# Kernel tuning notes

Measured on AMD Instinct MI355X. Metric: run time of the kernel, lower is better.

## Reference

```python
import jax, jax.numpy as jnp
import numpy as np

N = 10000      # nodes
E = 160000     # edges
B = 16         # graphs in batch
F_NODE = 42
F_EDGE = 12
D = 256        # hidden_dim
H = 4          # heads
C = D // H     # per-head channels = 64
L = 5          # num_layers
NEG_SLOPE = 0.2  # GATConv leaky_relu slope


def layernorm(x, g, b, eps=1e-5):
    mu = jnp.mean(x, axis=-1, keepdims=True)
    var = jnp.var(x, axis=-1, keepdims=True)
    return (x - mu) * jax.lax.rsqrt(var + eps) * g + b


def setup_inputs() -> dict:
    key = jax.random.key(0)
    ks = jax.random.split(key, 20)
    def w(i, shape, scale=0.05):
        return jax.random.normal(ks[i], shape, dtype=jnp.float32) * scale
    return {
        "x": jax.random.normal(ks[0], (N, F_NODE), dtype=jnp.float32),
        "edge_attr": jax.random.normal(ks[1], (E, F_EDGE), dtype=jnp.float32),
        "edge_index": jax.random.randint(ks[2], (2, E), 0, N),
        "batch": jnp.sort(jax.random.randint(ks[3], (N,), 0, B)),
        # node / edge encoders
        "enc_w": w(4, (F_NODE, D)), "enc_b": jnp.zeros((D,), jnp.float32),
        "eenc_w": w(5, (F_EDGE, D)), "eenc_b": jnp.zeros((D,), jnp.float32),
        # stacked GAT layer params [L, ...]
        "gat_w": w(6, (L, D, D)),          # lin_src == lin_dst (shared in PyG for Tensor input)
        "att_src": w(7, (L, H, C)),
        "att_dst": w(8, (L, H, C)),
        "att_edge": w(9, (L, H, C)),
        "gat_ew": w(10, (L, D, D)),        # lin_edge
        "gat_b": jnp.zeros((L, D), jnp.float32),
        "ln_g": jnp.ones((L, D), jnp.float32),
        "ln_b": jnp.zeros((L, D), jnp.float32),
        # attention pooling gate MLP
        "gate_w1": w(11, (D, D)), "gate_b1": jnp.zeros((D,), jnp.float32),
        "gate_w2": w(12, (D, 1)), "gate_b2": jnp.zeros((1,), jnp.float32),
        # MLP readout (mlp_layers=2)
        "ro_w1": w(13, (D, D)), "ro_b1": jnp.zeros((D,), jnp.float32),
        "ro_w2": w(14, (D, D)), "ro_b2": jnp.zeros((D,), jnp.float32),
    }


def reference(x, edge_index, edge_attr, batch, enc_w, enc_b, eenc_w, eenc_b,
              gat_w, att_src, att_dst, att_edge, gat_ew, gat_b, ln_g, ln_b,
              gate_w1, gate_b1, gate_w2, gate_b2, ro_w1, ro_b1, ro_w2, ro_b2):
    src0, dst0 = edge_index[0], edge_index[1]

    # encoders (dropout is identity at eval)
    h = jax.nn.relu(x @ enc_w + enc_b)                      # [N, D]
    e = jax.nn.relu(edge_attr @ eenc_w + eenc_b)            # [E, D]

    # GATConv add_self_loops with fill_value='mean': self-loop edge feature is
    # the mean of incoming edge features per destination node.
    esum = jax.ops.segment_sum(e, dst0, num_segments=N)
    cnt = jax.ops.segment_sum(jnp.ones((E,), e.dtype), dst0, num_segments=N)
    e_self = esum / jnp.maximum(cnt, 1.0)[:, None]
    e_full = jnp.concatenate([e, e_self], axis=0)           # [E+N, D]
    loops = jnp.arange(N)
    src = jnp.concatenate([src0, loops])
    dst = jnp.concatenate([dst0, loops])

    for l in range(L):
        xh = (h @ gat_w[l]).reshape(N, H, C)                # [N, H, C]
        a_s = jnp.einsum('nhc,hc->nh', xh, att_src[l])      # [N, H]
        a_d = jnp.einsum('nhc,hc->nh', xh, att_dst[l])
        eh = (e_full @ gat_ew[l]).reshape(-1, H, C)         # [E+N, H, C]
        a_e = jnp.einsum('ehc,hc->eh', eh, att_edge[l])
        alpha = jax.nn.leaky_relu(a_s[src] + a_d[dst] + a_e, NEG_SLOPE)  # [E+N, H]
        # softmax over incoming edges per destination node (stable)
        m = jax.lax.stop_gradient(jax.ops.segment_max(alpha, dst, num_segments=N))
        ex = jnp.exp(alpha - m[dst])
        den = jax.ops.segment_sum(ex, dst, num_segments=N)
        attn = ex / den[dst]                                # [E+N, H]
        msg = xh[src] * attn[:, :, None]                    # [E+N, H, C]
        out = jax.ops.segment_sum(msg, dst, num_segments=N).reshape(N, D) + gat_b[l]
        out = jax.nn.relu(layernorm(out, ln_g[l], ln_b[l]))
        h = h + out                                         # residual

    # GlobalAttention pooling: softmax(gate_nn(h)) per graph, weighted sum
    gate = (jax.nn.relu(h @ gate_w1 + gate_b1) @ gate_w2 + gate_b2)[:, 0]  # [N]
    gm = jax.lax.stop_gradient(jax.ops.segment_max(gate, batch, num_segments=B))
    ge = jnp.exp(gate - gm[batch])
    gd = jax.ops.segment_sum(ge, batch, num_segments=B)
    wgt = ge / gd[batch]
    g_embed = jax.ops.segment_sum(h * wgt[:, None], batch, num_segments=B)  # [B, D]

    # MLP readout
    return jax.nn.relu(g_embed @ ro_w1 + ro_b1) @ ro_w2 + ro_b2  # [B, D]
```

## Files before the change

### kernel.cpp

```cpp
#include <hip/hip_runtime.h>
#include <math.h>

#define DD 256
#define HH 4
#define CC 64
#define LL 5
#define NEG_SLOPE 0.2f
#define LH 20
#define WCAP 192

typedef __bf16 bf16x8 __attribute__((ext_vector_type(8)));
typedef __bf16 bf16x4 __attribute__((ext_vector_type(4)));
typedef float f32x4 __attribute__((ext_vector_type(4)));

static __device__ __forceinline__ float lrelu(float x) {
    return x > 0.0f ? x : NEG_SLOPE * x;
}

__global__ __launch_bounds__(256) void wproj_kernel(
    const float* __restrict__ gat_ew, const float* __restrict__ att_edge,
    float* __restrict__ wproj) {
    int l = blockIdx.x;
    int k = threadIdx.x;
    const float* W = gat_ew + (size_t)l * DD * DD;
    const float* att = att_edge + l * DD;
    for (int hh = 0; hh < HH; ++hh) {
        float s = 0.f;
        #pragma unroll
        for (int c = 0; c < CC; ++c)
            s += W[k * DD + hh * CC + c] * att[hh * CC + c];
        wproj[k * LH + l * HH + hh] = s;
    }
}

__global__ __launch_bounds__(256) void pack_edge_frags_kernel(
    const float* __restrict__ eenc_w, const float* __restrict__ eenc_b,
    const float* __restrict__ wproj, __bf16* __restrict__ wfe,
    __bf16* __restrict__ wfp) {
    int tid = threadIdx.x;
    for (int idx = tid; idx < 16 * 64; idx += 256) {
        int t = idx >> 6, lane = idx & 63;
        int q = lane >> 4, r15 = lane & 15;
        int col = t * 16 + r15;
        #pragma unroll
        for (int j = 0; j < 8; ++j) {
            int k = q * 8 + j;
            float v = (k < 12) ? eenc_w[k * 256 + col]
                               : (k == 12 ? eenc_b[col] : 0.f);
            wfe[(size_t)idx * 8 + j] = (__bf16)v;
        }
    }
    for (int idx = tid; idx < 16 * 64; idx += 256) {
        int sidx = idx >> 6, lane = idx & 63;
        int s = sidx >> 1, t2 = sidx & 1;
        int q = lane >> 4, r15 = lane & 15;
        int col = t2 * 16 + r15;
        #pragma unroll
        for (int j = 0; j < 8; ++j) {
            int k = s * 32 + q * 8 + j;
            float v = (col < LH) ? wproj[k * LH + col] : 0.f;
            wfp[(size_t)idx * 8 + j] = (__bf16)v;
        }
    }
}

__global__ __launch_bounds__(256) void wswizzle_kernel(
    const float* __restrict__ gat_w, const float* __restrict__ gate_w1,
    __bf16* __restrict__ wf) {
    int b = blockIdx.x;
    int l = b >> 5;
    int rem = b & 31;
    int y = rem >> 3, ks = rem & 7;
    int tid = threadIdx.x;
    int t = tid >> 6, lane = tid & 63;
    int q = lane >> 4, r15 = lane & 15;
    const float* W = (l < 5) ? (gat_w + (size_t)l * DD * DD) : gate_w1;
    size_t obase = (((size_t)b * 4 + t) * 64 + lane) * 8;
    int kbase = ks * 32 + q * 8;
    int col = y * 64 + t * 16 + r15;
    #pragma unroll
    for (int j = 0; j < 8; ++j)
        wf[obase + j] = (__bf16)W[(size_t)(kbase + j) * DD + col];
}

__global__ __launch_bounds__(256) void encoder_kernel(
    const float* __restrict__ x, const float* __restrict__ enc_w,
    const float* __restrict__ enc_b, float* __restrict__ h,
    __bf16* __restrict__ hbf, int N) {
    int n = blockIdx.x;
    int tid = threadIdx.x;
    __shared__ float xs[42];
    if (tid < 42) xs[tid] = x[(size_t)n * 42 + tid];
    __syncthreads();
    float acc = enc_b[tid];
    #pragma unroll
    for (int f = 0; f < 42; ++f) acc += xs[f] * enc_w[f * DD + tid];
    float v = fmaxf(acc, 0.f);
    h[(size_t)n * DD + tid] = v;
    hbf[(size_t)n * DD + tid] = (__bf16)v;
}

__global__ __launch_bounds__(256) void edge_mfma_kernel(
    const float* __restrict__ edge_attr, const __bf16* __restrict__ wfe,
    const __bf16* __restrict__ wfp, const int* __restrict__ pos,
    float* __restrict__ a_e_csr, int E) {
    __shared__ __bf16 sm[4][16][264];
    int tid = threadIdx.x;
    int w = tid >> 6, lane = tid & 63;
    int q = lane >> 4, r15 = lane & 15;
    int eb = blockIdx.x * 64 + w * 16;
    int e = eb + r15;
    int ec = min(e, E - 1);
    bf16x8 a1;
    #pragma unroll
    for (int j = 0; j < 8; ++j) a1[j] = (__bf16)0.f;
    if (q == 0) {
        const float4* p = (const float4*)(edge_attr + (size_t)ec * 12);
        float4 p0 = p[0], p1 = p[1];
        a1[0] = (__bf16)p0.x; a1[1] = (__bf16)p0.y; a1[2] = (__bf16)p0.z; a1[3] = (__bf16)p0.w;
        a1[4] = (__bf16)p1.x; a1[5] = (__bf16)p1.y; a1[6] = (__bf16)p1.z; a1[7] = (__bf16)p1.w;
    } else if (q == 1) {
        float4 p2 = *(const float4*)(edge_attr + (size_t)ec * 12 + 8);
        a1[0] = (__bf16)p2.x; a1[1] = (__bf16)p2.y; a1[2] = (__bf16)p2.z; a1[3] = (__bf16)p2.w;
        a1[4] = (__bf16)1.0f;
    }
    const bf16x8* wfeP = (const bf16x8*)wfe;
    f32x4 zero = (f32x4){0.f, 0.f, 0.f, 0.f};
    #pragma unroll
    for (int t = 0; t < 16; ++t) {
        bf16x8 bfr = wfeP[t * 64 + lane];
        f32x4 c = __builtin_amdgcn_mfma_f32_16x16x32_bf16(a1, bfr, zero, 0, 0, 0);
        int col = t * 16 + r15;
        #pragma unroll
        for (int r = 0; r < 4; ++r)
            sm[w][q * 4 + r][col] = (__bf16)fmaxf(c[r], 0.f);
    }
    const bf16x8* wfpP = (const bf16x8*)wfp;
    f32x4 c2[2];
    c2[0] = zero; c2[1] = zero;
    #pragma unroll
    for (int s = 0; s < 8; ++s) {
        bf16x8 a2 = *(const bf16x8*)&sm[w][r15][s * 32 + q * 8];
        #pragma unroll
        for (int t2 = 0; t2 < 2; ++t2)
            c2[t2] = __builtin_amdgcn_mfma_f32_16x16x32_bf16(
                a2, wfpP[(s * 2 + t2) * 64 + lane], c2[t2], 0, 0, 0);
    }
    #pragma unroll
    for (int t2 = 0; t2 < 2; ++t2) {
        int col = t2 * 16 + r15;
        if (col >= LH) continue;
        #pragma unroll
        for (int r = 0; r < 4; ++r) {
            int e2 = eb + q * 4 + r;
            if (e2 < E) {
                int pk = pos[e2];
                a_e_csr[(size_t)pk * LH + col] = c2[t2][r];
            }
        }
    }
}

__global__ void deg_kernel(const int* __restrict__ dst, int* __restrict__ deg, int E) {
    int e = blockIdx.x * 256 + threadIdx.x;
    if (e < E) atomicAdd(&deg[dst[e]], 1);
}

__global__ void self_ae_kernel(const int* __restrict__ row_ptr,
                               float* __restrict__ a_e_csr, int N, int E) {
    int i = blockIdx.x * 256 + threadIdx.x;
    if (i >= N * LH) return;
    int n = i / LH;
    int j = i % LH;
    int rs = row_ptr[n], re = row_ptr[n + 1];
    float s = 0.f;
    for (int k = rs; k < re; ++k)
        s += a_e_csr[(size_t)k * LH + j];
    a_e_csr[(size_t)(E + n) * LH + j] = s / (float)max(re - rs, 1);
}

__global__ __launch_bounds__(1024) void scan_kernel(const int* __restrict__ deg,
                                                    int* __restrict__ row_ptr,
                                                    int* __restrict__ cursor, int n) {
    __shared__ int wsum[16];
    __shared__ int carry_s;
    int tid = threadIdx.x;
    int w = tid >> 6, lane = tid & 63;
    if (tid == 0) carry_s = 0;
    __syncthreads();
    for (int base = 0; base < n; base += 1024) {
        int i = base + tid;
        int v = (i < n) ? deg[i] : 0;
        int carry = carry_s;
        int s = v;
        #pragma unroll
        for (int off = 1; off < 64; off <<= 1) {
            int t = __shfl_up(s, off, 64);
            if (lane >= off) s += t;
        }
        if (lane == 63) wsum[w] = s;
        __syncthreads();
        if (w == 0 && lane < 16) {
            int ws = wsum[lane];
            #pragma unroll
            for (int off = 1; off < 16; off <<= 1) {
                int t = __shfl_up(ws, off, 64);
                if (lane >= off) ws += t;
            }
            wsum[lane] = ws;
        }
        __syncthreads();
        int waveoff = (w == 0) ? 0 : wsum[w - 1];
        if (i < n) {
            int ex = carry + waveoff + s - v;
            row_ptr[i] = ex;
            cursor[i] = ex;
        }
        __syncthreads();
        if (tid == 0) carry_s = carry + wsum[15];
        __syncthreads();
    }
    if (tid == 0) row_ptr[n] = carry_s;
}

__global__ void scatter_kernel(const int* __restrict__ src, const int* __restrict__ dst,
                               int* __restrict__ cursor, int* __restrict__ csr_src,
                               int* __restrict__ pos, int E) {
    int e = blockIdx.x * 256 + threadIdx.x;
    if (e >= E) return;
    int d = dst[e];
    int pk = atomicAdd(&cursor[d], 1);
    csr_src[pk] = src[e];
    pos[e] = pk;
}

__global__ __launch_bounds__(256) void gemm_mfma_kernel(
    const __bf16* __restrict__ hbf, const __bf16* __restrict__ wf,
    __bf16* __restrict__ xhbf, int M,
    const float* __restrict__ att_src, const float* __restrict__ att_dst,
    float* __restrict__ a_s, float* __restrict__ a_d,
    const float* __restrict__ bias, const float* __restrict__ gate_w2,
    const float* __restrict__ gate_b2, float* __restrict__ gate_out) {
    int tid = threadIdx.x;
    int w = tid >> 6, lane = tid & 63;
    int q = lane >> 4, r15 = lane & 15;
    int m0 = blockIdx.x * 64;
    int y2 = blockIdx.y;
    int arow = m0 + w * 16 + r15;
    int arowc = min(arow, M - 1);
    const __bf16* ap = hbf + (size_t)arowc * DD + q * 8;
    const bf16x8* wfP = (const bf16x8*)wf;
    f32x4 acc[8];
    #pragma unroll
    for (int g = 0; g < 8; ++g) acc[g] = (f32x4){0.f, 0.f, 0.f, 0.f};
    #pragma unroll
    for (int ks = 0; ks < 8; ++ks) {
        bf16x8 a = *(const bf16x8*)(ap + ks * 32);
        #pragma unroll
        for (int g = 0; g < 8; ++g) {
            int y = y2 * 2 + (g >> 2);
            int t = g & 3;
            bf16x8 b = wfP[(size_t)(((y * 8 + ks) * 4) + t) * 64 + lane];
            acc[g] = __builtin_amdgcn_mfma_f32_16x16x32_bf16(a, b, acc[g], 0, 0, 0);
        }
    }
    if (xhbf) {
        #pragma unroll
        for (int g = 0; g < 8; ++g) {
            int col = (y2 * 8 + g) * 16 + r15;
            #pragma unroll
            for (int r = 0; r < 4; ++r) {
                int rc = m0 + w * 16 + q * 4 + r;
                if (rc < M) xhbf[(size_t)rc * DD + col] = (__bf16)acc[g][r];
            }
        }
    }
    if (att_src) {
        #pragma unroll
        for (int r = 0; r < 4; ++r) {
            float ps0 = 0.f, pd0 = 0.f, ps1 = 0.f, pd1 = 0.f;
            #pragma unroll
            for (int g = 0; g < 8; ++g) {
                int col = (y2 * 8 + g) * 16 + r15;
                float v = acc[g][r];
                if (g < 4) { ps0 += v * att_src[col]; pd0 += v * att_dst[col]; }
                else       { ps1 += v * att_src[col]; pd1 += v * att_dst[col]; }
            }
            #pragma unroll
            for (int mask = 1; mask < 16; mask <<= 1) {
                ps0 += __shfl_xor(ps0, mask, 64);
                pd0 += __shfl_xor(pd0, mask, 64);
                ps1 += __shfl_xor(ps1, mask, 64);
                pd1 += __shfl_xor(pd1, mask, 64);
            }
            int rc = m0 + w * 16 + q * 4 + r;
            if (r15 == 0 && rc < M) {
                a_s[rc * HH + y2 * 2 + 0] = ps0;
                a_d[rc * HH + y2 * 2 + 0] = pd0;
                a_s[rc * HH + y2 * 2 + 1] = ps1;
                a_d[rc * HH + y2 * 2 + 1] = pd1;
            }
        }
    }
    if (gate_w2) {
        #pragma unroll
        for (int r = 0; r < 4; ++r) {
            float pg = 0.f;
            #pragma unroll
            for (int g = 0; g < 8; ++g) {
                int col = (y2 * 8 + g) * 16 + r15;
                pg += fmaxf(acc[g][r] + bias[col], 0.f) * gate_w2[col];
            }
            #pragma unroll
            for (int mask = 1; mask < 16; mask <<= 1) pg += __shfl_xor(pg, mask, 64);
            int rc = m0 + w * 16 + q * 4 + r;
            if (r15 == 0 && rc < M) {
                float add = pg + (y2 == 0 ? gate_b2[0] : 0.f);
                atomicAdd(&gate_out[rc], add);
            }
        }
    }
}

__global__ __launch_bounds__(256) void gat_message7_kernel(
    const __bf16* __restrict__ xhbf, const float* __restrict__ a_s,
    const float* __restrict__ a_d, const float* __restrict__ a_e,
    const int* __restrict__ row_ptr, const int* __restrict__ csr_src,
    const float* __restrict__ gat_b,
    const float* __restrict__ ln_g, const float* __restrict__ ln_b,
    float* __restrict__ h, __bf16* __restrict__ hbf, int N, int E) {
    __shared__ float lws[4][WCAP * 4];
    __shared__ int lsrc[4][WCAP];
    int tid = threadIdx.x;
    int w = tid >> 6, lane = tid & 63;
    int n = blockIdx.x * 4 + w;
    if (n >= N) return;
    int hh = lane >> 4, j = lane & 15;
    int rs = row_ptr[n], re = row_ptr[n + 1];
    int deg = re - rs;
    float adn = a_d[n * HH + hh];
    float al_self = lrelu(a_s[n * HH + hh] + adn + a_e[(size_t)(E + n) * LH + hh]);
    float m = al_self, den = 0.f;
    for (int k = rs + j; k < re; k += 16) {
        int kk = k - rs;
        int s = csr_src[k];
        float a = lrelu(a_s[s * HH + hh] + adn + a_e[(size_t)k * LH + hh]);
        if (kk < WCAP) {
            lws[w][kk * 4 + hh] = a;
            if (hh == 0) lsrc[w][kk] = s;
        }
        float mn = fmaxf(m, a);
        den = den * __expf(m - mn) + __expf(a - mn);
        m = mn;
    }
    #pragma unroll
    for (int off = 1; off < 16; off <<= 1) {
        float m2 = __shfl_xor(m, off, 64);
        float d2 = __shfl_xor(den, off, 64);
        float mn = fmaxf(m, m2);
        den = den * __expf(m - mn) + d2 * __expf(m2 - mn);
        m = mn;
    }
    den += __expf(al_self - m);
    float inv_den = 1.0f / den;
    int cap = min(deg, WCAP);
    for (int kk = j; kk < cap; kk += 16)
        lws[w][kk * 4 + hh] = __expf(lws[w][kk * 4 + hh] - m) * inv_den;
    float wself = __expf(al_self - m) * inv_den;
    bf16x4 xsb = *((const bf16x4*)(xhbf + (size_t)n * DD) + lane);
    float4 acc;
    acc.x = wself * (float)xsb[0]; acc.y = wself * (float)xsb[1];
    acc.z = wself * (float)xsb[2]; acc.w = wself * (float)xsb[3];
    int k = rs;
    for (; k + 1 < re; k += 2) {
        int kk0 = k - rs, kk1 = kk0 + 1;
        int s0, s1_;
        float w0, w1;
        if (kk1 < WCAP) {
            s0 = lsrc[w][kk0]; s1_ = lsrc[w][kk1];
            w0 = lws[w][kk0 * 4 + hh]; w1 = lws[w][kk1 * 4 + hh];
        } else {
            s0 = csr_src[k]; s1_ = csr_src[k + 1];
            w0 = (kk0 < WCAP) ? lws[w][kk0 * 4 + hh]
               : __expf(lrelu(a_s[s0 * HH + hh] + adn + a_e[(size_t)k * LH + hh]) - m) * inv_den;
            w1 = __expf(lrelu(a_s[s1_ * HH + hh] + adn + a_e[(size_t)(k + 1) * LH + hh]) - m) * inv_den;
        }
        bf16x4 x0 = *((const bf16x4*)(xhbf + (size_t)s0 * DD) + lane);
        bf16x4 x1 = *((const bf16x4*)(xhbf + (size_t)s1_ * DD) + lane);
        acc.x += w0 * (float)x0[0] + w1 * (float)x1[0];
        acc.y += w0 * (float)x0[1] + w1 * (float)x1[1];
        acc.z += w0 * (float)x0[2] + w1 * (float)x1[2];
        acc.w += w0 * (float)x0[3] + w1 * (float)x1[3];
    }
    if (k < re) {
        int kk0 = k - rs;
        int s0;
        float w0;
        if (kk0 < WCAP) { s0 = lsrc[w][kk0]; w0 = lws[w][kk0 * 4 + hh]; }
        else {
            s0 = csr_src[k];
            w0 = __expf(lrelu(a_s[s0 * HH + hh] + adn + a_e[(size_t)k * LH + hh]) - m) * inv_den;
        }
        bf16x4 x0 = *((const bf16x4*)(xhbf + (size_t)s0 * DD) + lane);
        acc.x += w0 * (float)x0[0]; acc.y += w0 * (float)x0[1];
        acc.z += w0 * (float)x0[2]; acc.w += w0 * (float)x0[3];
    }
    float4 gb = *((const float4*)gat_b + lane);
    float4 val;
    val.x = acc.x + gb.x; val.y = acc.y + gb.y;
    val.z = acc.z + gb.z; val.w = acc.w + gb.w;
    float s1 = val.x + val.y + val.z + val.w;
    float s2 = val.x * val.x + val.y * val.y + val.z * val.z + val.w * val.w;
    #pragma unroll
    for (int off = 1; off < 64; off <<= 1) {
        s1 += __shfl_xor(s1, off, 64);
        s2 += __shfl_xor(s2, off, 64);
    }
    float mu = s1 * (1.0f / DD);
    float var = s2 * (1.0f / DD) - mu * mu;
    float rstd = rsqrtf(var + 1e-5f);
    float4 lg = *((const float4*)ln_g + lane);
    float4 lb = *((const float4*)ln_b + lane);
    float4 nv;
    nv.x = fmaxf((val.x - mu) * rstd * lg.x + lb.x, 0.f);
    nv.y = fmaxf((val.y - mu) * rstd * lg.y + lb.y, 0.f);
    nv.z = fmaxf((val.z - mu) * rstd * lg.z + lb.z, 0.f);
    nv.w = fmaxf((val.w - mu) * rstd * lg.w + lb.w, 0.f);
    float4* hp = (float4*)(h + (size_t)n * DD) + lane;
    float4 hv = *hp;
    hv.x += nv.x; hv.y += nv.y; hv.z += nv.z; hv.w += nv.w;
    *hp = hv;
    bf16x4 hb;
    hb[0] = (__bf16)hv.x; hb[1] = (__bf16)hv.y;
    hb[2] = (__bf16)hv.z; hb[3] = (__bf16)hv.w;
    *((bf16x4*)(hbf + (size_t)n * DD) + lane) = hb;
}

__global__ __launch_bounds__(256) void gseg_kernel(
    const float* __restrict__ gate, const int* __restrict__ batch,
    float* __restrict__ gmax, float* __restrict__ gden, int N) {
    int b = blockIdx.x;
    int tid = threadIdx.x;
    __shared__ int bounds[2];
    if (tid < 2) {
        int target = b + tid;
        int lo = 0, hi = N;
        while (lo < hi) {
            int mid = (lo + hi) >> 1;
            if (batch[mid] < target) lo = mid + 1; else hi = mid;
        }
        bounds[tid] = lo;
    }
    __syncthreads();
    int s0 = bounds[0], s1 = bounds[1];
    __shared__ float red[256];
    float m = -1e30f;
    for (int i = s0 + tid; i < s1; i += 256) m = fmaxf(m, gate[i]);
    red[tid] = m;
    __syncthreads();
    for (int off = 128; off; off >>= 1) {
        if (tid < off) red[tid] = fmaxf(red[tid], red[tid + off]);
        __syncthreads();
    }
    float gm = red[0];
    __syncthreads();
    float s = 0.f;
    for (int i = s0 + tid; i < s1; i += 256) s += __expf(gate[i] - gm);
    red[tid] = s;
    __syncthreads();
    for (int off = 128; off; off >>= 1) {
        if (tid < off) red[tid] += red[tid + off];
        __syncthreads();
    }
    if (tid == 0) {
        gmax[b] = gm;
        gden[b] = red[0];
    }
}

#define POOL_CHUNK 32
__global__ __launch_bounds__(256) void pool_scatter_kernel(
    const float* __restrict__ h, const float* __restrict__ gate,
    const float* __restrict__ gmax, const float* __restrict__ gden,
    const int* __restrict__ batch, float* __restrict__ g_embed, int N) {
    int i0 = blockIdx.x * POOL_CHUNK;
    int d = threadIdx.x;
    int iend = min(i0 + POOL_CHUNK, N);
    float acc = 0.f;
    int cur = batch[i0];
    for (int i = i0; i < iend; ++i) {
        int b = batch[i];
        if (b != cur) {
            atomicAdd(&g_embed[cur * DD + d], acc);
            acc = 0.f;
            cur = b;
        }
        float wgt = __expf(gate[i] - gmax[b]) / gden[b];
        acc += wgt * h[(size_t)i * DD + d];
    }
    atomicAdd(&g_embed[cur * DD + d], acc);
}

__global__ __launch_bounds__(256) void readout_kernel(
    const float* __restrict__ g_embed, const float* __restrict__ w1,
    const float* __restrict__ b1, const float* __restrict__ w2,
    const float* __restrict__ b2, float* __restrict__ out) {
    int b = blockIdx.x;
    int tid = threadIdx.x;
    __shared__ float gvec[256];
    __shared__ float hid[256];
    gvec[tid] = g_embed[b * DD + tid];
    __syncthreads();
    float hv = b1[tid];
    for (int k = 0; k < DD; ++k) hv += gvec[k] * w1[k * DD + tid];
    hid[tid] = fmaxf(hv, 0.f);
    __syncthreads();
    float o = b2[tid];
    for (int t = 0; t < DD; ++t) o += hid[t] * w2[t * DD + tid];
    out[b * DD + tid] = o;
}

extern "C" void kernel_launch(void* const* d_in, const int* in_sizes, int n_in,
                              void* d_out, int out_size, void* d_ws, size_t ws_size,
                              hipStream_t stream) {
    const float* x        = (const float*)d_in[0];
    const float* edge_attr= (const float*)d_in[1];
    const int*   edge_idx = (const int*)d_in[2];
    const int*   batch    = (const int*)d_in[3];
    const float* enc_w    = (const float*)d_in[4];
    const float* enc_b    = (const float*)d_in[5];
    const float* eenc_w   = (const float*)d_in[6];
    const float* eenc_b   = (const float*)d_in[7];
    const float* gat_w    = (const float*)d_in[8];
    const float* att_src  = (const float*)d_in[9];
    const float* att_dst  = (const float*)d_in[10];
    const float* att_edge = (const float*)d_in[11];
    const float* gat_ew   = (const float*)d_in[12];
    const float* gat_b    = (const float*)d_in[13];
    const float* ln_g     = (const float*)d_in[14];
    const float* ln_b     = (const float*)d_in[15];
    const float* gate_w1  = (const float*)d_in[16];
    const float* gate_b1  = (const float*)d_in[17];
    const float* gate_w2  = (const float*)d_in[18];
    const float* gate_b2  = (const float*)d_in[19];
    const float* ro_w1    = (const float*)d_in[20];
    const float* ro_b1    = (const float*)d_in[21];
    const float* ro_w2    = (const float*)d_in[22];
    const float* ro_b2    = (const float*)d_in[23];
    float* out = (float*)d_out;

    const int N = in_sizes[0] / 42;
    const int E = in_sizes[1] / 12;
    const int B = out_size / DD;

    char* p = (char*)d_ws;
    auto alloc = [&](size_t bytes) {
        char* r = p;
        p += (bytes + 255) & ~(size_t)255;
        return (void*)r;
    };
    float*  h       = (float*)alloc((size_t)N * DD * 4);
    __bf16* hbf     = (__bf16*)alloc((size_t)N * DD * 2);
    __bf16* xhbf    = (__bf16*)alloc((size_t)N * DD * 2);
    float*  a_s     = (float*)alloc((size_t)N * HH * 4);
    float*  a_d     = (float*)alloc((size_t)N * HH * 4);
    float*  a_e_csr = (float*)alloc((size_t)(E + N) * LH * 4);
    float*  wproj   = (float*)alloc((size_t)DD * LH * 4);
    __bf16* wfe     = (__bf16*)alloc((size_t)16 * 64 * 8 * 2);
    __bf16* wfp     = (__bf16*)alloc((size_t)16 * 64 * 8 * 2);
    __bf16* wf      = (__bf16*)alloc((size_t)6 * DD * DD * 2);
    float*  gate    = (float*)alloc((size_t)N * 4);
    float*  g_embed = (float*)alloc((size_t)B * DD * 4);
    float*  gmax    = (float*)alloc((size_t)B * 4);
    float*  gden    = (float*)alloc((size_t)B * 4);
    int* deg        = (int*)alloc((size_t)N * 4);
    int* row_ptr    = (int*)alloc((size_t)(N + 1) * 4);
    int* cursor     = (int*)alloc((size_t)N * 4);
    int* csr_src    = (int*)alloc((size_t)E * 4);
    int* pos        = (int*)alloc((size_t)E * 4);

    const int* src_arr = edge_idx;
    const int* dst_arr = edge_idx + E;

    hipMemsetAsync(deg, 0, (size_t)N * 4, stream);
    hipMemsetAsync(g_embed, 0, (size_t)B * DD * 4, stream);
    hipMemsetAsync(gate, 0, (size_t)N * 4, stream);

    wproj_kernel<<<LL, 256, 0, stream>>>(gat_ew, att_edge, wproj);
    pack_edge_frags_kernel<<<1, 256, 0, stream>>>(eenc_w, eenc_b, wproj, wfe, wfp);
    wswizzle_kernel<<<192, 256, 0, stream>>>(gat_w, gate_w1, wf);
    encoder_kernel<<<N, 256, 0, stream>>>(x, enc_w, enc_b, h, hbf, N);
    deg_kernel<<<(E + 255) / 256, 256, 0, stream>>>(dst_arr, deg, E);
    scan_kernel<<<1, 1024, 0, stream>>>(deg, row_ptr, cursor, N);
    scatter_kernel<<<(E + 255) / 256, 256, 0, stream>>>(
        src_arr, dst_arr, cursor, csr_src, pos, E);
    edge_mfma_kernel<<<(E + 63) / 64, 256, 0, stream>>>(
        edge_attr, wfe, wfp, pos, a_e_csr, E);
    self_ae_kernel<<<(N * LH + 255) / 256, 256, 0, stream>>>(
        row_ptr, a_e_csr, N, E);

    dim3 ggrid((N + 63) / 64, 2);
    for (int l = 0; l < LL; ++l) {
        gemm_mfma_kernel<<<ggrid, 256, 0, stream>>>(
            hbf, wf + (size_t)l * DD * DD, xhbf, N,
            att_src + l * DD, att_dst + l * DD, a_s, a_d,
            nullptr, nullptr, nullptr, nullptr);
        gat_message7_kernel<<<(N + 3) / 4, 256, 0, stream>>>(
            xhbf, a_s, a_d, a_e_csr + l * HH, row_ptr, csr_src,
            gat_b + l * DD, ln_g + l * DD, ln_b + l * DD, h, hbf, N, E);
    }

    gemm_mfma_kernel<<<ggrid, 256, 0, stream>>>(
        hbf, wf + (size_t)5 * DD * DD, nullptr, N,
        nullptr, nullptr, nullptr, nullptr,
        gate_b1, gate_w2, gate_b2, gate);
    gseg_kernel<<<B, 256, 0, stream>>>(gate, batch, gmax, gden, N);
    pool_scatter_kernel<<<(N + POOL_CHUNK - 1) / POOL_CHUNK, 256, 0, stream>>>(
        h, gate, gmax, gden, batch, g_embed, N);
    readout_kernel<<<B, 256, 0, stream>>>(g_embed, ro_w1, ro_b1, ro_w2, ro_b2, out);
}
```

Baseline: 428.7 us.

## Merge independent setup kernels into one mega launch and fuse scan with packing

Combines wproj, weight swizzle, degree counting, node encoder and two memsets into a single kernel that dispatches work by block index. Also folds the edge-fragment packing into a second block of the scan kernel. The aim is to cut launch overhead and the serialization gaps between small setup kernels. The trade-off is branch-heavy block dispatch, and the encoder path now uses __syncthreads inside a divergent-by-block branch, which is safe because it diverges per block.

```diff
diff --git a/kernel.cpp b/kernel.cpp
--- a/kernel.cpp
+++ b/kernel.cpp
@@ -17,87 +17,164 @@
     return x > 0.0f ? x : NEG_SLOPE * x;
 }
 
-__global__ __launch_bounds__(256) void wproj_kernel(
+__global__ __launch_bounds__(256) void mega_setup_kernel(
     const float* __restrict__ gat_ew, const float* __restrict__ att_edge,
-    float* __restrict__ wproj) {
-    int l = blockIdx.x;
-    int k = threadIdx.x;
-    const float* W = gat_ew + (size_t)l * DD * DD;
-    const float* att = att_edge + l * DD;
-    for (int hh = 0; hh < HH; ++hh) {
-        float s = 0.f;
-        #pragma unroll
-        for (int c = 0; c < CC; ++c)
-            s += W[k * DD + hh * CC + c] * att[hh * CC + c];
-        wproj[k * LH + l * HH + hh] = s;
-    }
-}
-
-__global__ __launch_bounds__(256) void pack_edge_frags_kernel(
+    float* __restrict__ wproj,
+    const float* __restrict__ gat_w, const float* __restrict__ gate_w1,
+    __bf16* __restrict__ wf,
+    const int* __restrict__ dst_arr, int* __restrict__ deg,
+    const float* __restrict__ x, const float* __restrict__ enc_w,
+    const float* __restrict__ enc_b, float* __restrict__ h,
+    __bf16* __restrict__ hbf,
+    float* __restrict__ g_embed, float* __restrict__ gate_out,
+    int N, int E, int B) {
+    int blk = blockIdx.x;
+    int tid = threadIdx.x;
+    int EB = (E + 255) >> 8;
+    if (blk < 5) {
+        int l = blk;
+        int k = tid;
+        const float* W = gat_ew + (size_t)l * DD * DD;
+        const float* att = att_edge + l * DD;
+        for (int hh = 0; hh < HH; ++hh) {
+            float s = 0.f;
+            #pragma unroll
+            for (int c = 0; c < CC; ++c)
+                s += W[k * DD + hh * CC + c] * att[hh * CC + c];
+            wproj[k * LH + l * HH + hh] = s;
+        }
+        return;
+    }
+    blk -= 5;
+    if (blk < 192) {
+        int b = blk;
+        int l = b >> 5;
+        int rem = b & 31;
+        int y = rem >> 3, ks = rem & 7;
+        int t = tid >> 6, lane = tid & 63;
+        int q = lane >> 4, r15 = lane & 15;
+        const float* W = (l < 5) ? (gat_w + (size_t)l * DD * DD) : gate_w1;
+        size_t obase = (((size_t)b * 4 + t) * 64 + lane) * 8;
+        int kbase = ks * 32 + q * 8;
+        int col = y * 64 + t * 16 + r15;
+        #pragma unroll
+        for (int j = 0; j < 8; ++j)
+            wf[obase + j] = (__bf16)W[(size_t)(kbase + j) * DD + col];
+        return;
+    }
+    blk -= 192;
+    if (blk < EB) {
+        int e = blk * 256 + tid;
+        if (e < E) atomicAdd(&deg[dst_arr[e]], 1);
+        return;
+    }
+    blk -= EB;
+    if (blk < N) {
+        int n = blk;
+        __shared__ float xs[42];
+        if (tid < 42) xs[tid] = x[(size_t)n * 42 + tid];
+        __syncthreads();
+        float acc = enc_b[tid];
+        #pragma unroll
+        for (int f = 0; f < 42; ++f) acc += xs[f] * enc_w[f * DD + tid];
+        float v = fmaxf(acc, 0.f);
+        h[(size_t)n * DD + tid] = v;
+        hbf[(size_t)n * DD + tid] = (__bf16)v;
+        return;
+    }
+    blk -= N;
+    if (blk == 0) {
+        for (int i = tid; i < B * DD; i += 256) g_embed[i] = 0.f;
+        return;
+    }
+    for (int i = tid; i < N; i += 256) gate_out[i] = 0.f;
+}
+
+__global__ __launch_bounds__(1024) void scan_pack_kernel(
+    const int* __restrict__ deg, int* __restrict__ row_ptr,
+    int* __restrict__ cursor, int n,
     const float* __restrict__ eenc_w, const float* __restrict__ eenc_b,
     const float* __restrict__ wproj, __bf16* __restrict__ wfe,
     __bf16* __restrict__ wfp) {
     int tid = threadIdx.x;
-    for (int idx = tid; idx < 16 * 64; idx += 256) {
-        int t = idx >> 6, lane = idx & 63;
-        int q = lane >> 4, r15 = lane & 15;
-        int col = t * 16 + r15;
-        #pragma unroll
-        for (int j = 0; j < 8; ++j) {
-            int k = q * 8 + j;
-            float v = (k < 12) ? eenc_w[k * 256 + col]
-                               : (k == 12 ? eenc_b[col] : 0.f);
-            wfe[(size_t)idx * 8 + j] = (__bf16)v;
-        }
-    }
-    for (int idx = tid; idx < 16 * 64; idx += 256) {
-        int sidx = idx >> 6, lane = idx & 63;
-        int s = sidx >> 1, t2 = sidx & 1;
-        int q = lane >> 4, r15 = lane & 15;
-        int col = t2 * 16 + r15;
-        #pragma unroll
-        for (int j = 0; j < 8; ++j) {
-            int k = s * 32 + q * 8 + j;
-            float v = (col < LH) ? wproj[k * LH + col] : 0.f;
-            wfp[(size_t)idx * 8 + j] = (__bf16)v;
-        }
-    }
-}
-
-__global__ __launch_bounds__(256) void wswizzle_kernel(
-    const float* __restrict__ gat_w, const float* __restrict__ gate_w1,
-    __bf16* __restrict__ wf) {
-    int b = blockIdx.x;
-    int l = b >> 5;
-    int rem = b & 31;
-    int y = rem >> 3, ks = rem & 7;
-    int tid = threadIdx.x;
-    int t = tid >> 6, lane = tid & 63;
-    int q = lane >> 4, r15 = lane & 15;
-    const float* W = (l < 5) ? (gat_w + (size_t)l * DD * DD) : gate_w1;
-    size_t obase = (((size_t)b * 4 + t) * 64 + lane) * 8;
-    int kbase = ks * 32 + q * 8;
-    int col = y * 64 + t * 16 + r15;
-    #pragma unroll
-    for (int j = 0; j < 8; ++j)
-        wf[obase + j] = (__bf16)W[(size_t)(kbase + j) * DD + col];
-}
-
-__global__ __launch_bounds__(256) void encoder_kernel(
-    const float* __restrict__ x, const float* __restrict__ enc_w,
-    const float* __restrict__ enc_b, float* __restrict__ h,
-    __bf16* __restrict__ hbf, int N) {
-    int n = blockIdx.x;
-    int tid = threadIdx.x;
-    __shared__ float xs[42];
-    if (tid < 42) xs[tid] = x[(size_t)n * 42 + tid];
+    if (blockIdx.x == 1) {
+        {
+            int idx = tid;
+            int t = idx >> 6, lane = idx & 63;
+            int q = lane >> 4, r15 = lane & 15;
+            int col = t * 16 + r15;
+            #pragma unroll
+            for (int j = 0; j < 8; ++j) {
+                int k = q * 8 + j;
+                float v = (k < 12) ? eenc_w[k * 256 + col]
+                                   : (k == 12 ? eenc_b[col] : 0.f);
+                wfe[(size_t)idx * 8 + j] = (__bf16)v;
+            }
+        }
+        {
+            int idx = tid;
+            int sidx = idx >> 6, lane = idx & 63;
+            int s = sidx >> 1, t2 = sidx & 1;
+            int q = lane >> 4, r15 = lane & 15;
+            int col = t2 * 16 + r15;
+            #pragma unroll
+            for (int j = 0; j < 8; ++j) {
+                int k = s * 32 + q * 8 + j;
+                float v = (col < LH) ? wproj[k * LH + col] : 0.f;
+                wfp[(size_t)idx * 8 + j] = (__bf16)v;
+            }
+        }
+        return;
+    }
+    __shared__ int wsum[16];
+    __shared__ int carry_s;
+    int w = tid >> 6, lane = tid & 63;
+    if (tid == 0) carry_s = 0;
     __syncthreads();
-    float acc = enc_b[tid];
-    #pragma unroll
-    for (int f = 0; f < 42; ++f) acc += xs[f] * enc_w[f * DD + tid];
-    float v = fmaxf(acc, 0.f);
-    h[(size_t)n * DD + tid] = v;
-    hbf[(size_t)n * DD + tid] = (__bf16)v;
+    for (int base = 0; base < n; base += 1024) {
+        int i = base + tid;
+        int v = (i < n) ? deg[i] : 0;
+        int carry = carry_s;
+        int s = v;
+        #pragma unroll
+        for (int off = 1; off < 64; off <<= 1) {
+            int t = __shfl_up(s, off, 64);
+            if (lane >= off) s += t;
+        }
+        if (lane == 63) wsum[w] = s;
+        __syncthreads();
+        if (w == 0 && lane < 16) {
+            int ws = wsum[lane];
+            #pragma unroll
+            for (int off = 1; off < 16; off <<= 1) {
+                int t = __shfl_up(ws, off, 64);
+                if (lane >= off) ws += t;
+            }
+            wsum[lane] = ws;
+        }
+        __syncthreads();
+        int waveoff = (w == 0) ? 0 : wsum[w - 1];
+        if (i < n) {
+            int ex = carry + waveoff + s - v;
+            row_ptr[i] = ex;
+            cursor[i] = ex;
+        }
+        __syncthreads();
+        if (tid == 0) carry_s = carry + wsum[15];
+        __syncthreads();
+    }
+    if (tid == 0) row_ptr[n] = carry_s;
+}
+
+__global__ void scatter_kernel(const int* __restrict__ src, const int* __restrict__ dst,
+                               int* __restrict__ cursor, int* __restrict__ csr_src,
+                               int* __restrict__ pos, int E) {
+    int e = blockIdx.x * 256 + threadIdx.x;
+    if (e >= E) return;
+    int d = dst[e];
+    int pk = atomicAdd(&cursor[d], 1);
+    csr_src[pk] = src[e];
+    pos[e] = pk;
 }
 
 __global__ __launch_bounds__(256) void edge_mfma_kernel(
@@ -161,11 +238,6 @@
     }
 }
 
-__global__ void deg_kernel(const int* __restrict__ dst, int* __restrict__ deg, int E) {
-    int e = blockIdx.x * 256 + threadIdx.x;
-    if (e < E) atomicAdd(&deg[dst[e]], 1);
-}
-
 __global__ void self_ae_kernel(const int* __restrict__ row_ptr,
                                float* __restrict__ a_e_csr, int N, int E) {
     int i = blockIdx.x * 256 + threadIdx.x;
@@ -177,61 +249,6 @@
     for (int k = rs; k < re; ++k)
         s += a_e_csr[(size_t)k * LH + j];
     a_e_csr[(size_t)(E + n) * LH + j] = s / (float)max(re - rs, 1);
-}
-
-__global__ __launch_bounds__(1024) void scan_kernel(const int* __restrict__ deg,
-                                                    int* __restrict__ row_ptr,
-                                                    int* __restrict__ cursor, int n) {
-    __shared__ int wsum[16];
-    __shared__ int carry_s;
-    int tid = threadIdx.x;
-    int w = tid >> 6, lane = tid & 63;
-    if (tid == 0) carry_s = 0;
-    __syncthreads();
-    for (int base = 0; base < n; base += 1024) {
-        int i = base + tid;
-        int v = (i < n) ? deg[i] : 0;
-        int carry = carry_s;
-        int s = v;
-        #pragma unroll
-        for (int off = 1; off < 64; off <<= 1) {
-            int t = __shfl_up(s, off, 64);
-            if (lane >= off) s += t;
-        }
-        if (lane == 63) wsum[w] = s;
-        __syncthreads();
-        if (w == 0 && lane < 16) {
-            int ws = wsum[lane];
-            #pragma unroll
-            for (int off = 1; off < 16; off <<= 1) {
-                int t = __shfl_up(ws, off, 64);
-                if (lane >= off) ws += t;
-            }
-            wsum[lane] = ws;
-        }
-        __syncthreads();
-        int waveoff = (w == 0) ? 0 : wsum[w - 1];
-        if (i < n) {
-            int ex = carry + waveoff + s - v;
-            row_ptr[i] = ex;
-            cursor[i] = ex;
-        }
-        __syncthreads();
-        if (tid == 0) carry_s = carry + wsum[15];
-        __syncthreads();
-    }
-    if (tid == 0) row_ptr[n] = carry_s;
-}
-
-__global__ void scatter_kernel(const int* __restrict__ src, const int* __restrict__ dst,
-                               int* __restrict__ cursor, int* __restrict__ csr_src,
-                               int* __restrict__ pos, int E) {
-    int e = blockIdx.x * 256 + threadIdx.x;
-    if (e >= E) return;
-    int d = dst[e];
-    int pk = atomicAdd(&cursor[d], 1);
-    csr_src[pk] = src[e];
-    pos[e] = pk;
 }
 
 __global__ __launch_bounds__(256) void gemm_mfma_kernel(
@@ -583,15 +600,14 @@
     const int* dst_arr = edge_idx + E;
 
     hipMemsetAsync(deg, 0, (size_t)N * 4, stream);
-    hipMemsetAsync(g_embed, 0, (size_t)B * DD * 4, stream);
-    hipMemsetAsync(gate, 0, (size_t)N * 4, stream);
-
-    wproj_kernel<<<LL, 256, 0, stream>>>(gat_ew, att_edge, wproj);
-    pack_edge_frags_kernel<<<1, 256, 0, stream>>>(eenc_w, eenc_b, wproj, wfe, wfp);
-    wswizzle_kernel<<<192, 256, 0, stream>>>(gat_w, gate_w1, wf);
-    encoder_kernel<<<N, 256, 0, stream>>>(x, enc_w, enc_b, h, hbf, N);
-    deg_kernel<<<(E + 255) / 256, 256, 0, stream>>>(dst_arr, deg, E);
-    scan_kernel<<<1, 1024, 0, stream>>>(deg, row_ptr, cursor, N);
+
+    const int EB = (E + 255) / 256;
+    int mega_grid = 5 + 192 + EB + N + 2;
+    mega_setup_kernel<<<mega_grid, 256, 0, stream>>>(
+        gat_ew, att_edge, wproj, gat_w, gate_w1, wf,
+        dst_arr, deg, x, enc_w, enc_b, h, hbf, g_embed, gate, N, E, B);
+    scan_pack_kernel<<<2, 1024, 0, stream>>>(
+        deg, row_ptr, cursor, N, eenc_w, eenc_b, wproj, wfe, wfp);
     scatter_kernel<<<(E + 255) / 256, 256, 0, stream>>>(
         src_arr, dst_arr, cursor, csr_src, pos, E);
     edge_mfma_kernel<<<(E + 63) / 64, 256, 0, stream>>>(
```

Result: faster. 402.6 us (-6.1%).
